# Optimization experiments

Hardware: AMD Instinct MI355X
Metric: run time of the kernel (lower is better)

## Reference

```python
import jax, jax.numpy as jnp
import numpy as np

N, H, DH = 8, 12, 64          # batch, heads, head dim (embedding_dim=768)
LV, LA = 1568, 512            # video / audio token counts
NCV, NCA = 392, 256           # candidates kept: LV*(1-0.75), LA*(1-0.5)
SCALE = DH ** -0.5            # avmatching_module.scale


def setup_inputs() -> dict:
    key = jax.random.key(0)
    ks = jax.random.split(key, 14)
    f32 = jnp.float32
    return {
        "pos_v_q": jax.random.normal(ks[0], (N, H, LV, DH), f32),
        "pos_v_k": jax.random.normal(ks[1], (N, H, LV, DH), f32),
        "pos_a_q": jax.random.normal(ks[2], (N, H, LA, DH), f32),
        "pos_a_k": jax.random.normal(ks[3], (N, H, LA, DH), f32),
        "pos_cross_att_av": jax.random.uniform(ks[4], (N, H, LA, LV), f32),
        "pos_cross_att_va": jax.random.uniform(ks[5], (N, H, LV, LA), f32),
        "n_attn_av": jax.random.uniform(ks[6], (N, LV), f32, 0.01, 1.0),
        "n_attn_va": jax.random.uniform(ks[7], (N, LA), f32, 0.01, 1.0),
        "spu_a_cls": jax.random.normal(ks[8], (N, H, DH), f32),
        "spu_v_cls": jax.random.normal(ks[9], (N, H, DH), f32),
        "u_v": jax.random.uniform(ks[10], (N, LV), f32),
        "u_a": jax.random.uniform(ks[11], (N, LA), f32),
        # att ids come from argsort of attention scores in the original -> permutations
        "att_av_ids": jnp.argsort(jax.random.uniform(ks[12], (N, LV)), axis=1),
        "att_va_ids": jnp.argsort(jax.random.uniform(ks[13], (N, LA)), axis=1),
    }


def _pipeline(pos_v_q, pos_v_k, pos_a_q, pos_a_k, pos_cross_att_av, pos_cross_att_va,
              n_attn_av, n_attn_va, spu_a_cls, spu_v_cls, u_v, u_a,
              att_av_ids, att_va_ids):
    idx_v = att_av_ids[:, :NCV]   # kept video token ids
    idx_a = att_va_ids[:, :NCA]   # kept audio token ids

    # --- gather kept tokens (torch.gather dim=2) and attention-weighted cls pooling ---
    d_v_k = jnp.take_along_axis(pos_v_k, idx_v[:, None, :, None], axis=2)   # [N,H,NCV,DH]
    v_tok = jnp.take_along_axis(pos_v_q, idx_v[:, None, :, None], axis=2)
    d_n_av = jnp.take_along_axis(n_attn_av, idx_v, axis=1)                  # [N,NCV]
    pos_v_cls = jnp.einsum('nhld,nl->nhd', v_tok, d_n_av) / jnp.sum(d_n_av, 1)[:, None, None]

    d_a_k = jnp.take_along_axis(pos_a_k, idx_a[:, None, :, None], axis=2)   # [N,H,NCA,DH]
    a_tok = jnp.take_along_axis(pos_a_q, idx_a[:, None, :, None], axis=2)
    d_n_va = jnp.take_along_axis(n_attn_va, idx_a, axis=1)                  # [N,NCA]
    pos_a_cls = jnp.einsum('nhld,nl->nhd', a_tok, d_n_va) / jnp.sum(d_n_va, 1)[:, None, None]

    # --- video keep probability: spurious (buffer audio query) vs positive attention ---
    v_spu = jnp.einsum('nhld,nhd->nhl', d_v_k, spu_a_cls) * SCALE           # [N,H,NCV]
    v_pos = jnp.take_along_axis(pos_cross_att_av, idx_v[:, None, None, :], axis=3)  # [N,H,LA,NCV]
    v_pos = jnp.take_along_axis(v_pos, idx_a[:, None, :, None], axis=2)     # [N,H,NCA,NCV]
    v_pos = jnp.einsum('nhal,na->nhl', v_pos, d_n_va) / jnp.sum(d_n_va, 1)[:, None, None]
    v_att = jax.nn.softmax(jnp.stack([v_spu, v_pos], axis=-1), axis=-1).mean(axis=1)
    prob_v = v_att[..., 0]                                                  # [N,NCV]
    restore_v = jnp.argsort(att_av_ids, axis=1)
    prob_v_full = jnp.take_along_axis(
        jnp.concatenate([prob_v, jnp.zeros((prob_v.shape[0], LV - NCV), prob_v.dtype)], axis=1),
        restore_v, axis=1)                                                  # [N,LV]

    # --- audio keep probability: spurious (buffer video query) vs positive attention ---
    a_spu = jnp.einsum('nhld,nhd->nhl', d_a_k, spu_v_cls) * SCALE           # [N,H,NCA]
    a_pos = jnp.take_along_axis(pos_cross_att_va, idx_a[:, None, None, :], axis=3)  # [N,H,LV,NCA]
    a_pos = jnp.take_along_axis(a_pos, idx_v[:, None, :, None], axis=2)     # [N,H,NCV,NCA]
    a_pos = jnp.einsum('nhvl,nv->nhl', a_pos, d_n_av) / jnp.sum(d_n_av, 1)[:, None, None]
    a_att = jax.nn.softmax(jnp.stack([a_spu, a_pos], axis=-1), axis=-1).mean(axis=1)
    prob_a = a_att[..., 0]                                                  # [N,NCA]
    restore_a = jnp.argsort(att_va_ids, axis=1)
    prob_a_full = jnp.take_along_axis(
        jnp.concatenate([prob_a, jnp.zeros((prob_a.shape[0], LA - NCA), prob_a.dtype)], axis=1),
        restore_a, axis=1)                                                  # [N,LA]

    # --- bernoulli pruning, deterministic via external uniforms (u < p == bernoulli(p)) ---
    prune_n_av = jnp.where(u_v < prob_v_full, 0.0, n_attn_av)
    prune_n_va = jnp.where(u_a < prob_a_full, 0.0, n_attn_va)

    n = prob_v_full.shape[0]
    return jnp.concatenate([prob_v_full, prob_a_full,
                            pos_v_cls.reshape(n, -1), pos_a_cls.reshape(n, -1),
                            prune_n_av, prune_n_va], axis=1)


def reference(pos_v_q, pos_v_k, pos_a_q, pos_a_k, pos_cross_att_av, pos_cross_att_va,
              n_attn_av, n_attn_va, spu_a_cls, spu_v_cls, u_v, u_a,
              att_av_ids, att_va_ids):
    return _pipeline(pos_v_q, pos_v_k, pos_a_q, pos_a_k, pos_cross_att_av,
                     pos_cross_att_va, n_attn_av, n_attn_va, spu_a_cls, spu_v_cls,
                     u_v, u_a, att_av_ids, att_va_ids)
```

## Files before the change

### kernel.cpp

```cpp
#include <hip/hip_runtime.h>

#define NN 8
#define HH 12
#define DH 64
#define LV 1568
#define LA 512
#define NCV 392
#define NCA 256
#define SCALE 0.125f

#define OUT_STRIDE (LV + LA + 2 * HH * DH + LV + LA)
#define OFF_PROB_V 0
#define OFF_PROB_A (LV)
#define OFF_VCLS   (LV + LA)
#define OFF_ACLS   (LV + LA + HH * DH)
#define OFF_PR_AV  (LV + LA + 2 * HH * DH)
#define OFF_PR_VA  (LV + LA + 2 * HH * DH + LV)

#define WS_RV      0
#define WS_RA      (NN * HH * LV)
#define WS_WAV     (WS_RA + NN * HH * LA)
#define WS_WVA     (WS_WAV + NN * NCV)
#define WS_INV_SAV (WS_WVA + NN * NCA)
#define WS_INV_SVA (WS_INV_SAV + NN)

#define CHA 8
#define CHV 8

__global__ void prep_kernel(const float* __restrict__ n_av,
                            const float* __restrict__ n_va,
                            const int* __restrict__ av_ids,
                            const int* __restrict__ va_ids,
                            float* __restrict__ ws) {
    int n = blockIdx.x;
    int t = threadIdx.x;
    int wave = t >> 6;

    float wv = 0.f, wa = 0.f;
    if (t < NCV) {
        wv = n_av[n * LV + av_ids[n * LV + t]];
        ws[WS_WAV + n * NCV + t] = wv;
    }
    if (t < NCA) {
        wa = n_va[n * LA + va_ids[n * LA + t]];
        ws[WS_WVA + n * NCA + t] = wa;
    }
    float vs = wv, as = wa;
    for (int m = 32; m; m >>= 1) { vs += __shfl_xor(vs, m); as += __shfl_xor(as, m); }
    __shared__ float sv[8], sa[8];
    if ((t & 63) == 0) { sv[wave] = vs; sa[wave] = as; }
    __syncthreads();
    if (t == 0) {
        float S0 = 0.f, S1 = 0.f;
        #pragma unroll
        for (int i = 0; i < 8; ++i) { S0 += sv[i]; S1 += sa[i]; }
        ws[WS_INV_SAV + n] = 1.f / S0;
        ws[WS_INV_SVA + n] = 1.f / S1;
    }
}

__global__ __launch_bounds__(256) void rowsum_kernel(
        const float* __restrict__ av,
        const float* __restrict__ va,
        const int* __restrict__ av_ids,
        const int* __restrict__ va_ids,
        float* __restrict__ ws) {
    int b = blockIdx.x;
    int t = threadIdx.x;
    if (b < NN * HH * CHA) {
        int chunk = b % CHA;
        int nh    = b / CHA;
        int n     = nh / HH;
        const int rows = NCA / CHA;
        float4 acc0 = {0.f, 0.f, 0.f, 0.f};
        float4 acc1 = {0.f, 0.f, 0.f, 0.f};
        const int c0 = t;
        const int c1 = t + 256;
        const bool has1 = (c1 < LV / 4);
        for (int r = 0; r < rows; ++r) {
            int a = chunk * rows + r;
            int ridx = va_ids[n * LA + a];
            float w  = ws[WS_WVA + n * NCA + a];
            const float4* row = (const float4*)(av + ((size_t)nh * LA + ridx) * LV);
            float4 x0 = row[c0];
            acc0.x += x0.x * w; acc0.y += x0.y * w; acc0.z += x0.z * w; acc0.w += x0.w * w;
            if (has1) {
                float4 x1 = row[c1];
                acc1.x += x1.x * w; acc1.y += x1.y * w; acc1.z += x1.z * w; acc1.w += x1.w * w;
            }
        }
        float* out = ws + WS_RV + (size_t)nh * LV;
        atomicAdd(&out[c0 * 4 + 0], acc0.x);
        atomicAdd(&out[c0 * 4 + 1], acc0.y);
        atomicAdd(&out[c0 * 4 + 2], acc0.z);
        atomicAdd(&out[c0 * 4 + 3], acc0.w);
        if (has1) {
            atomicAdd(&out[c1 * 4 + 0], acc1.x);
            atomicAdd(&out[c1 * 4 + 1], acc1.y);
            atomicAdd(&out[c1 * 4 + 2], acc1.z);
            atomicAdd(&out[c1 * 4 + 3], acc1.w);
        }
    } else {
        int b2    = b - NN * HH * CHA;
        int chunk = b2 % CHV;
        int nh    = b2 / CHV;
        int n     = nh / HH;
        const int rows = NCV / CHV;
        float2 acc = {0.f, 0.f};
        const int c = t;
        for (int r = 0; r < rows; ++r) {
            int v = chunk * rows + r;
            int ridx = av_ids[n * LV + v];
            float w  = ws[WS_WAV + n * NCV + v];
            const float2* row = (const float2*)(va + ((size_t)nh * LV + ridx) * LA);
            float2 x = row[c];
            acc.x += x.x * w; acc.y += x.y * w;
        }
        float* out = ws + WS_RA + (size_t)nh * LA;
        atomicAdd(&out[c * 2 + 0], acc.x);
        atomicAdd(&out[c * 2 + 1], acc.y);
    }
}

__global__ __launch_bounds__(256) void cls_kernel(
        const float* __restrict__ pvq,
        const float* __restrict__ paq,
        const int* __restrict__ av_ids,
        const int* __restrict__ va_ids,
        const float* __restrict__ ws,
        float* __restrict__ out) {
    int b = blockIdx.x;
    int t = threadIdx.x;
    int wave = t >> 6, lane = t & 63;
    __shared__ float red[4][DH];
    if (b < NN * HH) {
        int n = b / HH, h = b % HH;
        float acc = 0.f;
        for (int l = wave; l < NCV; l += 4) {
            int ridx = av_ids[n * LV + l];
            float w  = ws[WS_WAV + n * NCV + l];
            acc += pvq[((size_t)b * LV + ridx) * DH + lane] * w;
        }
        red[wave][lane] = acc;
        __syncthreads();
        if (wave == 0) {
            float s = red[0][lane] + red[1][lane] + red[2][lane] + red[3][lane];
            out[(size_t)n * OUT_STRIDE + OFF_VCLS + h * DH + lane] = s * ws[WS_INV_SAV + n];
        }
    } else {
        int b2 = b - NN * HH;
        int n = b2 / HH, h = b2 % HH;
        float acc = 0.f;
        for (int l = wave; l < NCA; l += 4) {
            int ridx = va_ids[n * LA + l];
            float w  = ws[WS_WVA + n * NCA + l];
            acc += paq[((size_t)b2 * LA + ridx) * DH + lane] * w;
        }
        red[wave][lane] = acc;
        __syncthreads();
        if (wave == 0) {
            float s = red[0][lane] + red[1][lane] + red[2][lane] + red[3][lane];
            out[(size_t)n * OUT_STRIDE + OFF_ACLS + h * DH + lane] = s * ws[WS_INV_SVA + n];
        }
    }
}

__global__ __launch_bounds__(256) void prob_kernel(
        const float* __restrict__ pvk,
        const float* __restrict__ pak,
        const float* __restrict__ spu_a,
        const float* __restrict__ spu_v,
        const int* __restrict__ av_ids,
        const int* __restrict__ va_ids,
        const float* __restrict__ ws,
        float* __restrict__ out) {
    int W = blockIdx.x * 4 + (threadIdx.x >> 6);
    int lane = threadIdx.x & 63;
    if (W < NN * NCV) {
        int n = W / NCV, l = W % NCV;
        int col = av_ids[n * LV + l];
        float invS = ws[WS_INV_SVA + n];
        float psum = 0.f;
        #pragma unroll
        for (int h = 0; h < HH; ++h) {
            int nh = n * HH + h;
            float prod = pvk[((size_t)nh * LV + col) * DH + lane] * spu_a[nh * DH + lane];
            for (int m = 32; m; m >>= 1) prod += __shfl_xor(prod, m);
            float spu = prod * SCALE;
            float pos = ws[WS_RV + (size_t)nh * LV + col] * invS;
            psum += 1.f / (1.f + __expf(pos - spu));
        }
        if (lane == 0)
            out[(size_t)n * OUT_STRIDE + OFF_PROB_V + col] = psum * (1.f / HH);
    } else if (W < NN * NCV + NN * NCA) {
        int W2 = W - NN * NCV;
        int n = W2 / NCA, l = W2 % NCA;
        int col = va_ids[n * LA + l];
        float invS = ws[WS_INV_SAV + n];
        float psum = 0.f;
        #pragma unroll
        for (int h = 0; h < HH; ++h) {
            int nh = n * HH + h;
            float prod = pak[((size_t)nh * LA + col) * DH + lane] * spu_v[nh * DH + lane];
            for (int m = 32; m; m >>= 1) prod += __shfl_xor(prod, m);
            float spu = prod * SCALE;
            float pos = ws[WS_RA + (size_t)nh * LA + col] * invS;
            psum += 1.f / (1.f + __expf(pos - spu));
        }
        if (lane == 0)
            out[(size_t)n * OUT_STRIDE + OFF_PROB_A + col] = psum * (1.f / HH);
    }
}

__global__ __launch_bounds__(256) void prune_kernel(
        const float* __restrict__ n_av,
        const float* __restrict__ n_va,
        const float* __restrict__ u_v,
        const float* __restrict__ u_a,
        float* __restrict__ out) {
    int t = blockIdx.x * 256 + threadIdx.x;
    const int total = NN * (LV + LA);
    if (t >= total) return;
    int n = t / (LV + LA);
    int j = t % (LV + LA);
    if (j < LV) {
        float prob = out[(size_t)n * OUT_STRIDE + OFF_PROB_V + j];
        float uv   = u_v[n * LV + j];
        out[(size_t)n * OUT_STRIDE + OFF_PR_AV + j] = (uv < prob) ? 0.f : n_av[n * LV + j];
    } else {
        int j2 = j - LV;
        float prob = out[(size_t)n * OUT_STRIDE + OFF_PROB_A + j2];
        float ua   = u_a[n * LA + j2];
        out[(size_t)n * OUT_STRIDE + OFF_PR_VA + j2] = (ua < prob) ? 0.f : n_va[n * LA + j2];
    }
}

extern "C" void kernel_launch(void* const* d_in, const int* in_sizes, int n_in,
                              void* d_out, int out_size, void* d_ws, size_t ws_size,
                              hipStream_t stream) {
    const float* pvq   = (const float*)d_in[0];
    const float* pvk   = (const float*)d_in[1];
    const float* paq   = (const float*)d_in[2];
    const float* pak   = (const float*)d_in[3];
    const float* av    = (const float*)d_in[4];
    const float* va    = (const float*)d_in[5];
    const float* n_av  = (const float*)d_in[6];
    const float* n_va  = (const float*)d_in[7];
    const float* spu_a = (const float*)d_in[8];
    const float* spu_v = (const float*)d_in[9];
    const float* u_v   = (const float*)d_in[10];
    const float* u_a   = (const float*)d_in[11];
    const int* av_ids  = (const int*)d_in[12];
    const int* va_ids  = (const int*)d_in[13];
    float* out = (float*)d_out;
    float* ws  = (float*)d_ws;

    hipMemsetAsync(d_out, 0, (size_t)out_size * sizeof(float), stream);
    hipMemsetAsync(d_ws, 0, (size_t)(NN * HH * LV + NN * HH * LA) * sizeof(float), stream);

    prep_kernel<<<NN, 512, 0, stream>>>(n_av, n_va, av_ids, va_ids, ws);
    rowsum_kernel<<<NN * HH * (CHA + CHV), 256, 0, stream>>>(av, va, av_ids, va_ids, ws);
    cls_kernel<<<2 * NN * HH, 256, 0, stream>>>(pvq, paq, av_ids, va_ids, ws, out);
    int waves = NN * NCV + NN * NCA;
    prob_kernel<<<(waves + 3) / 4, 256, 0, stream>>>(pvk, pak, spu_a, spu_v,
                                                     av_ids, va_ids, ws, out);
    prune_kernel<<<(NN * (LV + LA) + 255) / 256, 256, 0, stream>>>(n_av, n_va, u_v, u_a, out);
}
```

Baseline: 665.4 us.

## Fuse memsets, prep and prune into init and prob kernels

Replaces the two memsets and the prep kernel with one init kernel that zeroes the workspace with float4 stores and computes the inverse weight sums. The rowsum and cls kernels now read the gathered weights directly from the input instead of a precomputed workspace copy, and the cls kernel computes its own normalizer. The prune step moves into the prob kernel, which now covers all token positions and writes zeros for non-candidates, so no output memset is needed. This cuts launch count and small passes, at the cost of some idle waves in prob_kernel.

```diff
diff --git a/kernel.cpp b/kernel.cpp
--- a/kernel.cpp
+++ b/kernel.cpp
@@ -19,43 +19,39 @@
 
 #define WS_RV      0
 #define WS_RA      (NN * HH * LV)
-#define WS_WAV     (WS_RA + NN * HH * LA)
-#define WS_WVA     (WS_WAV + NN * NCV)
-#define WS_INV_SAV (WS_WVA + NN * NCA)
+#define WS_INV_SAV (WS_RA + NN * HH * LA)
 #define WS_INV_SVA (WS_INV_SAV + NN)
 
 #define CHA 8
 #define CHV 8
 
-__global__ void prep_kernel(const float* __restrict__ n_av,
-                            const float* __restrict__ n_va,
-                            const int* __restrict__ av_ids,
-                            const int* __restrict__ va_ids,
-                            float* __restrict__ ws) {
-    int n = blockIdx.x;
+__global__ __launch_bounds__(256) void init_kernel(
+        const float* __restrict__ n_av,
+        const float* __restrict__ n_va,
+        const int* __restrict__ av_ids,
+        const int* __restrict__ va_ids,
+        float* __restrict__ ws) {
     int t = threadIdx.x;
-    int wave = t >> 6;
-
-    float wv = 0.f, wa = 0.f;
-    if (t < NCV) {
-        wv = n_av[n * LV + av_ids[n * LV + t]];
-        ws[WS_WAV + n * NCV + t] = wv;
-    }
-    if (t < NCA) {
-        wa = n_va[n * LA + va_ids[n * LA + t]];
-        ws[WS_WVA + n * NCA + t] = wa;
-    }
-    float vs = wv, as = wa;
-    for (int m = 32; m; m >>= 1) { vs += __shfl_xor(vs, m); as += __shfl_xor(as, m); }
-    __shared__ float sv[8], sa[8];
-    if ((t & 63) == 0) { sv[wave] = vs; sa[wave] = as; }
-    __syncthreads();
-    if (t == 0) {
-        float S0 = 0.f, S1 = 0.f;
-        #pragma unroll
-        for (int i = 0; i < 8; ++i) { S0 += sv[i]; S1 += sa[i]; }
-        ws[WS_INV_SAV + n] = 1.f / S0;
-        ws[WS_INV_SVA + n] = 1.f / S1;
+    int idx = blockIdx.x * 256 + t;
+    const int total4 = (NN * HH * LV + NN * HH * LA) / 4;
+    if (idx < total4) ((float4*)ws)[idx] = make_float4(0.f, 0.f, 0.f, 0.f);
+
+    if (blockIdx.x < NN) {
+        int n = blockIdx.x;
+        float vs = 0.f, as = 0.f;
+        for (int l = t; l < NCV; l += 256) vs += n_av[n * LV + av_ids[n * LV + l]];
+        if (t < NCA) as = n_va[n * LA + va_ids[n * LA + t]];
+        for (int m = 32; m; m >>= 1) { vs += __shfl_xor(vs, m); as += __shfl_xor(as, m); }
+        __shared__ float sv[4], sa[4];
+        int wave = t >> 6;
+        if ((t & 63) == 0) { sv[wave] = vs; sa[wave] = as; }
+        __syncthreads();
+        if (t == 0) {
+            float S0 = sv[0] + sv[1] + sv[2] + sv[3];
+            float S1 = sa[0] + sa[1] + sa[2] + sa[3];
+            ws[WS_INV_SAV + n] = 1.f / S0;
+            ws[WS_INV_SVA + n] = 1.f / S1;
+        }
     }
 }
 
@@ -64,6 +60,8 @@
         const float* __restrict__ va,
         const int* __restrict__ av_ids,
         const int* __restrict__ va_ids,
+        const float* __restrict__ n_av,
+        const float* __restrict__ n_va,
         float* __restrict__ ws) {
     int b = blockIdx.x;
     int t = threadIdx.x;
@@ -80,7 +78,7 @@
         for (int r = 0; r < rows; ++r) {
             int a = chunk * rows + r;
             int ridx = va_ids[n * LA + a];
-            float w  = ws[WS_WVA + n * NCA + a];
+            float w  = n_va[n * LA + ridx];
             const float4* row = (const float4*)(av + ((size_t)nh * LA + ridx) * LV);
             float4 x0 = row[c0];
             acc0.x += x0.x * w; acc0.y += x0.y * w; acc0.z += x0.z * w; acc0.w += x0.w * w;
@@ -111,7 +109,7 @@
         for (int r = 0; r < rows; ++r) {
             int v = chunk * rows + r;
             int ridx = av_ids[n * LV + v];
-            float w  = ws[WS_WAV + n * NCV + v];
+            float w  = n_av[n * LV + ridx];
             const float2* row = (const float2*)(va + ((size_t)nh * LV + ridx) * LA);
             float2 x = row[c];
             acc.x += x.x * w; acc.y += x.y * w;
@@ -127,40 +125,48 @@
         const float* __restrict__ paq,
         const int* __restrict__ av_ids,
         const int* __restrict__ va_ids,
-        const float* __restrict__ ws,
+        const float* __restrict__ n_av,
+        const float* __restrict__ n_va,
         float* __restrict__ out) {
     int b = blockIdx.x;
     int t = threadIdx.x;
     int wave = t >> 6, lane = t & 63;
     __shared__ float red[4][DH];
+    __shared__ float wred[4];
     if (b < NN * HH) {
         int n = b / HH, h = b % HH;
-        float acc = 0.f;
+        float acc = 0.f, wsum = 0.f;
         for (int l = wave; l < NCV; l += 4) {
             int ridx = av_ids[n * LV + l];
-            float w  = ws[WS_WAV + n * NCV + l];
-            acc += pvq[((size_t)b * LV + ridx) * DH + lane] * w;
+            float w  = n_av[n * LV + ridx];
+            acc  += pvq[((size_t)b * LV + ridx) * DH + lane] * w;
+            wsum += w;
         }
         red[wave][lane] = acc;
+        if (lane == 0) wred[wave] = wsum;
         __syncthreads();
         if (wave == 0) {
             float s = red[0][lane] + red[1][lane] + red[2][lane] + red[3][lane];
-            out[(size_t)n * OUT_STRIDE + OFF_VCLS + h * DH + lane] = s * ws[WS_INV_SAV + n];
+            float W = wred[0] + wred[1] + wred[2] + wred[3];
+            out[(size_t)n * OUT_STRIDE + OFF_VCLS + h * DH + lane] = s / W;
         }
     } else {
         int b2 = b - NN * HH;
         int n = b2 / HH, h = b2 % HH;
-        float acc = 0.f;
+        float acc = 0.f, wsum = 0.f;
         for (int l = wave; l < NCA; l += 4) {
             int ridx = va_ids[n * LA + l];
-            float w  = ws[WS_WVA + n * NCA + l];
-            acc += paq[((size_t)b2 * LA + ridx) * DH + lane] * w;
+            float w  = n_va[n * LA + ridx];
+            acc  += paq[((size_t)b2 * LA + ridx) * DH + lane] * w;
+            wsum += w;
         }
         red[wave][lane] = acc;
+        if (lane == 0) wred[wave] = wsum;
         __syncthreads();
         if (wave == 0) {
             float s = red[0][lane] + red[1][lane] + red[2][lane] + red[3][lane];
-            out[(size_t)n * OUT_STRIDE + OFF_ACLS + h * DH + lane] = s * ws[WS_INV_SVA + n];
+            float W = wred[0] + wred[1] + wred[2] + wred[3];
+            out[(size_t)n * OUT_STRIDE + OFF_ACLS + h * DH + lane] = s / W;
         }
     }
 }
@@ -172,66 +178,64 @@
         const float* __restrict__ spu_v,
         const int* __restrict__ av_ids,
         const int* __restrict__ va_ids,
+        const float* __restrict__ n_av,
+        const float* __restrict__ n_va,
+        const float* __restrict__ u_v,
+        const float* __restrict__ u_a,
         const float* __restrict__ ws,
         float* __restrict__ out) {
     int W = blockIdx.x * 4 + (threadIdx.x >> 6);
     int lane = threadIdx.x & 63;
-    if (W < NN * NCV) {
-        int n = W / NCV, l = W % NCV;
+    const int TV = NN * LV;
+    if (W < TV) {
+        int n = W / LV, l = W % LV;
         int col = av_ids[n * LV + l];
-        float invS = ws[WS_INV_SVA + n];
-        float psum = 0.f;
-        #pragma unroll
-        for (int h = 0; h < HH; ++h) {
-            int nh = n * HH + h;
-            float prod = pvk[((size_t)nh * LV + col) * DH + lane] * spu_a[nh * DH + lane];
-            for (int m = 32; m; m >>= 1) prod += __shfl_xor(prod, m);
-            float spu = prod * SCALE;
-            float pos = ws[WS_RV + (size_t)nh * LV + col] * invS;
-            psum += 1.f / (1.f + __expf(pos - spu));
-        }
-        if (lane == 0)
-            out[(size_t)n * OUT_STRIDE + OFF_PROB_V + col] = psum * (1.f / HH);
-    } else if (W < NN * NCV + NN * NCA) {
-        int W2 = W - NN * NCV;
-        int n = W2 / NCA, l = W2 % NCA;
+        float p = 0.f;
+        if (l < NCV) {
+            float invS = ws[WS_INV_SVA + n];
+            float psum = 0.f;
+            #pragma unroll
+            for (int h = 0; h < HH; ++h) {
+                int nh = n * HH + h;
+                float prod = pvk[((size_t)nh * LV + col) * DH + lane] * spu_a[nh * DH + lane];
+                for (int m = 32; m; m >>= 1) prod += __shfl_xor(prod, m);
+                float spu = prod * SCALE;
+                float pos = ws[WS_RV + (size_t)nh * LV + col] * invS;
+                psum += 1.f / (1.f + __expf(pos - spu));
+            }
+            p = psum * (1.f / HH);
+        }
+        if (lane == 0) {
+            out[(size_t)n * OUT_STRIDE + OFF_PROB_V + col] = p;
+            float uv = u_v[n * LV + col];
+            out[(size_t)n * OUT_STRIDE + OFF_PR_AV + col] =
+                (uv < p) ? 0.f : n_av[n * LV + col];
+        }
+    } else {
+        int W2 = W - TV;
+        int n = W2 / LA, l = W2 % LA;
         int col = va_ids[n * LA + l];
-        float invS = ws[WS_INV_SAV + n];
-        float psum = 0.f;
-        #pragma unroll
-        for (int h = 0; h < HH; ++h) {
-            int nh = n * HH + h;
-            float prod = pak[((size_t)nh * LA + col) * DH + lane] * spu_v[nh * DH + lane];
-            for (int m = 32; m; m >>= 1) prod += __shfl_xor(prod, m);
-            float spu = prod * SCALE;
-            float pos = ws[WS_RA + (size_t)nh * LA + col] * invS;
-            psum += 1.f / (1.f + __expf(pos - spu));
-        }
-        if (lane == 0)
-            out[(size_t)n * OUT_STRIDE + OFF_PROB_A + col] = psum * (1.f / HH);
-    }
-}
-
-__global__ __launch_bounds__(256) void prune_kernel(
-        const float* __restrict__ n_av,
-        const float* __restrict__ n_va,
-        const float* __restrict__ u_v,
-        const float* __restrict__ u_a,
-        float* __restrict__ out) {
-    int t = blockIdx.x * 256 + threadIdx.x;
-    const int total = NN * (LV + LA);
-    if (t >= total) return;
-    int n = t / (LV + LA);
-    int j = t % (LV + LA);
-    if (j < LV) {
-        float prob = out[(size_t)n * OUT_STRIDE + OFF_PROB_V + j];
-        float uv   = u_v[n * LV + j];
-        out[(size_t)n * OUT_STRIDE + OFF_PR_AV + j] = (uv < prob) ? 0.f : n_av[n * LV + j];
-    } else {
-        int j2 = j - LV;
-        float prob = out[(size_t)n * OUT_STRIDE + OFF_PROB_A + j2];
-        float ua   = u_a[n * LA + j2];
-        out[(size_t)n * OUT_STRIDE + OFF_PR_VA + j2] = (ua < prob) ? 0.f : n_va[n * LA + j2];
+        float p = 0.f;
+        if (l < NCA) {
+            float invS = ws[WS_INV_SAV + n];
+            float psum = 0.f;
+            #pragma unroll
+            for (int h = 0; h < HH; ++h) {
+                int nh = n * HH + h;
+                float prod = pak[((size_t)nh * LA + col) * DH + lane] * spu_v[nh * DH + lane];
+                for (int m = 32; m; m >>= 1) prod += __shfl_xor(prod, m);
+                float spu = prod * SCALE;
+                float pos = ws[WS_RA + (size_t)nh * LA + col] * invS;
+                psum += 1.f / (1.f + __expf(pos - spu));
+            }
+            p = psum * (1.f / HH);
+        }
+        if (lane == 0) {
+            out[(size_t)n * OUT_STRIDE + OFF_PROB_A + col] = p;
+            float ua = u_a[n * LA + col];
+            out[(size_t)n * OUT_STRIDE + OFF_PR_VA + col] =
+                (ua < p) ? 0.f : n_va[n * LA + col];
+        }
     }
 }
 
@@ -255,14 +259,12 @@
     float* out = (float*)d_out;
     float* ws  = (float*)d_ws;
 
-    hipMemsetAsync(d_out, 0, (size_t)out_size * sizeof(float), stream);
-    hipMemsetAsync(d_ws, 0, (size_t)(NN * HH * LV + NN * HH * LA) * sizeof(float), stream);
-
-    prep_kernel<<<NN, 512, 0, stream>>>(n_av, n_va, av_ids, va_ids, ws);
-    rowsum_kernel<<<NN * HH * (CHA + CHV), 256, 0, stream>>>(av, va, av_ids, va_ids, ws);
-    cls_kernel<<<2 * NN * HH, 256, 0, stream>>>(pvq, paq, av_ids, va_ids, ws, out);
-    int waves = NN * NCV + NN * NCA;
-    prob_kernel<<<(waves + 3) / 4, 256, 0, stream>>>(pvk, pak, spu_a, spu_v,
-                                                     av_ids, va_ids, ws, out);
-    prune_kernel<<<(NN * (LV + LA) + 255) / 256, 256, 0, stream>>>(n_av, n_va, u_v, u_a, out);
-}
+    init_kernel<<<256, 256, 0, stream>>>(n_av, n_va, av_ids, va_ids, ws);
+    rowsum_kernel<<<NN * HH * (CHA + CHV), 256, 0, stream>>>(av, va, av_ids, va_ids,
+                                                             n_av, n_va, ws);
+    cls_kernel<<<2 * NN * HH, 256, 0, stream>>>(pvq, paq, av_ids, va_ids,
+                                                n_av, n_va, out);
+    prob_kernel<<<NN * (LV + LA) / 4, 256, 0, stream>>>(pvk, pak, spu_a, spu_v,
+                                                        av_ids, va_ids, n_av, n_va,
+                                                        u_v, u_a, ws, out);
+}
```

Measured after the change: 645.2 us. -3.0%, faster.
